# Kernel tuning notes

Hardware: AMD Instinct MI355X
Metric: run time of the kernel (lower is better)

## Reference

```python
import jax, jax.numpy as jnp
import numpy as np

# dims
B, T = 256, 64
N_AG, N_FEAT = 10, 4
X_DIM, X_PERM, X_STATIC = 44, 40, 10
HID, XEMB, NHID = 128, 32, 8
E = N_AG * (N_AG - 1)           # 90 directed edges (off-diagonal)
GEMB = NHID * E                 # 720 graph embedding per sample/step
RNN_IN = XEMB + 1 + GEMB        # 753
A_IN = X_STATIC + GEMB          # 730 (x_emb_size2==0 in GraphNN branch)
O_IN = XEMB + X_STATIC + 1 + GEMB  # 763

_off = np.ones((N_AG, N_AG)) - np.eye(N_AG)
RECV = jnp.asarray(np.where(_off)[0])  # rel_rec one-hot == gather by receiver idx
SEND = jnp.asarray(np.where(_off)[1])  # rel_send one-hot == gather by sender idx


def setup_inputs() -> dict:
    key = jax.random.key(0)
    ks = jax.random.split(key, 32)
    w = lambda k, shape: jax.random.normal(k, shape, jnp.float32) * 0.05
    return {
        'x': jax.random.normal(ks[0], (B, T + 1, X_DIM), jnp.float32),
        'x_demo': jax.random.normal(ks[1], (B, X_STATIC), jnp.float32),
        'f_treatment': jax.random.uniform(ks[2], (B, T + 1, 1), jnp.float32),
        'h0': jax.random.normal(ks[3], (B, HID), jnp.float32),
        # x2emb (Linear 4->32), x_static2emb (Linear 10->10)
        'W_x2emb': w(ks[4], (XEMB, X_DIM - X_PERM)), 'b_x2emb': w(ks[5], (XEMB,)),
        'W_stat': w(ks[6], (X_STATIC, X_STATIC)), 'b_stat': w(ks[7], (X_STATIC,)),
        # NRI-style MLP1 (node): 4->8->8 ; MLP2 (edge): 16->8->8
        'W_m1a': w(ks[8], (NHID, N_FEAT)), 'b_m1a': w(ks[9], (NHID,)),
        'W_m1b': w(ks[10], (NHID, NHID)), 'b_m1b': w(ks[11], (NHID,)),
        'W_m2a': w(ks[12], (NHID, 2 * NHID)), 'b_m2a': w(ks[13], (NHID,)),
        'W_m2b': w(ks[14], (NHID, NHID)), 'b_m2b': w(ks[15], (NHID,)),
        # treatment head: Linear(730->128)+ReLU, then Linear(128->1, no bias)
        'W_a1': w(ks[16], (HID, A_IN)), 'b_a1': w(ks[17], (HID,)),
        'W_a2': w(ks[18], (1, HID)),
        # outcome head: Linear(763->128)+ReLU, then Linear(128->1, no bias)
        'W_o1': w(ks[19], (HID, O_IN)), 'b_o1': w(ks[20], (HID,)),
        'W_o2': w(ks[21], (1, HID)),
        # GRUCell(753 -> 128)
        'W_ih': w(ks[22], (3 * HID, RNN_IN)), 'b_ih': w(ks[23], (3 * HID,)),
        'W_hh': w(ks[24], (3 * HID, HID)), 'b_hh': w(ks[25], (3 * HID,)),
    }


def reference(x, x_demo, f_treatment, h0, W_x2emb, b_x2emb, W_stat, b_stat,
              W_m1a, b_m1a, W_m1b, b_m1b, W_m2a, b_m2a, W_m2b, b_m2b,
              W_a1, b_a1, W_a2, W_o1, b_o1, W_o2, W_ih, b_ih, W_hh, b_hh):
    xt = x[:, :T]                       # (B,T,44); len_time = x.size(1)-1
    treat = f_treatment[:, :T]          # (B,T,1)
    demo = x_demo @ W_stat.T + b_stat   # (B,10) static embedding
    demoT = jnp.broadcast_to(demo[:, None], (B, T, X_STATIC))

    # --- GNN(x_permuted): mlp1 per node, node2edge gather, mlp2 per edge ---
    xa = xt[..., :X_PERM].reshape(B, T, N_AG, N_FEAT)
    h1 = jax.nn.elu(xa @ W_m1a.T + b_m1a)
    h1 = jax.nn.elu(h1 @ W_m1b.T + b_m1b)         # (B,T,N_AG,8); BN in eval = identity
    edges = jnp.concatenate([h1[:, :, RECV], h1[:, :, SEND]], axis=-1)  # (B,T,E,16)
    h2 = jax.nn.elu(edges @ W_m2a.T + b_m2a)
    h2 = jax.nn.elu(h2 @ W_m2b.T + b_m2b)         # (B,T,E,8)
    gemb = h2.reshape(B, T, GEMB)                 # (B,T,720)

    xemb = xt[..., X_PERM:] @ W_x2emb.T + b_x2emb  # (B,T,32)

    # --- treatment (a_or_ipw) head; dropout identity in eval ---
    a_in = jnp.concatenate([demoT, gemb], axis=-1)          # (B,T,730)
    a_out = jax.nn.relu(a_in @ W_a1.T + b_a1) @ W_a2.T      # (B,T,1)

    # --- outcome head ---
    o_in = jnp.concatenate([xemb, demoT, treat, gemb], axis=-1)  # (B,T,763)
    y_out = jax.nn.relu(o_in @ W_o1.T + b_o1) @ W_o2.T           # (B,T,1)

    # --- GRUCell recurrence over time ---
    rnn_in = jnp.concatenate([xemb, treat, gemb], axis=-1)  # (B,T,753)
    gi = rnn_in @ W_ih.T + b_ih                             # precompute input proj (B,T,3H)

    def step(h, g):
        gh = h @ W_hh.T + b_hh
        i_r, i_z, i_n = jnp.split(g, 3, axis=-1)
        h_r, h_z, h_n = jnp.split(gh, 3, axis=-1)
        r = jax.nn.sigmoid(i_r + h_r)
        z = jax.nn.sigmoid(i_z + h_z)
        n = jnp.tanh(i_n + r * h_n)
        h_new = (1.0 - z) * n + z * h
        return h_new, h_new

    _, hs = jax.lax.scan(step, h0, jnp.swapaxes(gi, 0, 1))
    hs = jnp.swapaxes(hs, 0, 1)                             # (B,T,128)

    return jnp.concatenate([a_out, y_out, hs], axis=-1)     # (B,T,130)
```

## Files before the change

kernel.cpp:

```cpp
#include <hip/hip_runtime.h>
#include <hip/hip_bf16.h>
#include <math.h>

#define BB     256
#define TT     64
#define BT     (BB*TT)
#define XD     44
#define XP     40
#define XS     10
#define HID    128
#define XEMB   32
#define NHID   8
#define NAG    10
#define NEDGE  90
#define GEMB   720
#define KF     768
#define NTOT   640


typedef __bf16  bf16_t;
typedef __bf16  bf16x4 __attribute__((ext_vector_type(4)));
typedef __bf16  bf16x8 __attribute__((ext_vector_type(8)));
typedef float   floatx4 __attribute__((ext_vector_type(4)));
typedef _Float16 half2_t __attribute__((ext_vector_type(2)));
typedef _Float16 half4_t __attribute__((ext_vector_type(4)));
typedef _Float16 half8_t __attribute__((ext_vector_type(8)));

__device__ __forceinline__ float rcp_fast(float x) { return __builtin_amdgcn_rcpf(x); }
__device__ __forceinline__ float sigmoid_fast(float v) { return rcp_fast(1.f + __expf(-v)); }
__device__ __forceinline__ float tanh_fast(float x) { return 1.f - 2.f * rcp_fast(1.f + __expf(2.f * x)); }
__device__ __forceinline__ float elu_fast(float v) { return v > 0.f ? v : __expf(v) - 1.f; }
__device__ __forceinline__ float fdot2f(half2_t a, half2_t b, float acc) {
  return __builtin_amdgcn_fdot2(a, b, acc, false);
}
__device__ __forceinline__ float dot8h(half8_t a, half8_t b, float acc) {
  acc = fdot2f(half2_t{a[0], a[1]}, half2_t{b[0], b[1]}, acc);
  acc = fdot2f(half2_t{a[2], a[3]}, half2_t{b[2], b[3]}, acc);
  acc = fdot2f(half2_t{a[4], a[5]}, half2_t{b[4], b[5]}, acc);
  acc = fdot2f(half2_t{a[6], a[7]}, half2_t{b[6], b[7]}, acc);
  return acc;
}
__device__ __forceinline__ void lds_barrier() {
  asm volatile("s_waitcnt lgkmcnt(0)" ::: "memory");
  __builtin_amdgcn_s_barrier();
}

__global__ __launch_bounds__(256) void prep_kernel(
    const float* __restrict__ Wa1, const float* __restrict__ ba1,
    const float* __restrict__ Wo1, const float* __restrict__ bo1,
    const float* __restrict__ Wih, const float* __restrict__ bih,
    bf16_t* __restrict__ WT, float* __restrict__ bcat) {
  int idx = blockIdx.x * 256 + threadIdx.x;
  if (idx >= NTOT * KF) return;
  int n = idx / KF, k = idx - n * KF;
  float v = 0.f;
  if (n < 128) {
    if (k >= 32 && k < 42)  v = Wa1[n * 730 + (k - 32)];
    else if (k >= 48)       v = Wa1[n * 730 + 10 + (k - 48)];
  } else if (n < 256) {
    int m = n - 128;
    if (k < 43)             v = Wo1[m * 763 + k];
    else if (k >= 48)       v = Wo1[m * 763 + 43 + (k - 48)];
  } else {
    int m = n - 256;
    if (k < 32)             v = Wih[m * 753 + k];
    else if (k == 42)       v = Wih[m * 753 + 32];
    else if (k >= 48)       v = Wih[m * 753 + 33 + (k - 48)];
  }
  WT[n * KF + k] = (bf16_t)v;
  if (k == 0) {
    bcat[n] = (n < 128) ? ba1[n] : (n < 256 ? bo1[n - 128] : bih[n - 256]);
  }
}

__global__ __launch_bounds__(64) void encoder_kernel(
    const float* __restrict__ x, const float* __restrict__ x_demo,
    const float* __restrict__ ftreat,
    const float* __restrict__ Wm1a, const float* __restrict__ bm1a,
    const float* __restrict__ Wm1b, const float* __restrict__ bm1b,
    const float* __restrict__ Wm2a, const float* __restrict__ bm2a,
    const float* __restrict__ Wm2b, const float* __restrict__ bm2b,
    const float* __restrict__ Wx2e, const float* __restrict__ bx2e,
    const float* __restrict__ Wst, const float* __restrict__ bst,
    bf16_t* __restrict__ F) {
  int blk = blockIdx.x;
  int b = blk >> 4, tc = blk & 15;
  int lane = threadIdx.x;

  __shared__ __align__(16) _Float16 h1sp[NAG * 8];
  __shared__ __align__(16) _Float16 w2aR[64];
  __shared__ __align__(16) _Float16 w2aS[64];
  __shared__ __align__(16) _Float16 w2bp[64];
  __shared__ float demoL[XS];

  if (lane < 8) {
    float4 v0 = *(const float4*)(Wm2a + lane * 16);
    float4 v1 = *(const float4*)(Wm2a + lane * 16 + 4);
    float4 v2 = *(const float4*)(Wm2a + lane * 16 + 8);
    float4 v3 = *(const float4*)(Wm2a + lane * 16 + 12);
    *(half8_t*)&w2aR[lane * 8] = half8_t{
        (_Float16)v0.x, (_Float16)v0.y, (_Float16)v0.z, (_Float16)v0.w,
        (_Float16)v1.x, (_Float16)v1.y, (_Float16)v1.z, (_Float16)v1.w};
    *(half8_t*)&w2aS[lane * 8] = half8_t{
        (_Float16)v2.x, (_Float16)v2.y, (_Float16)v2.z, (_Float16)v2.w,
        (_Float16)v3.x, (_Float16)v3.y, (_Float16)v3.z, (_Float16)v3.w};
    float4 u0 = *(const float4*)(Wm2b + lane * 8);
    float4 u1 = *(const float4*)(Wm2b + lane * 8 + 4);
    *(half8_t*)&w2bp[lane * 8] = half8_t{
        (_Float16)u0.x, (_Float16)u0.y, (_Float16)u0.z, (_Float16)u0.w,
        (_Float16)u1.x, (_Float16)u1.y, (_Float16)u1.z, (_Float16)u1.w};
  }
  if (lane < 10) {
    float s = bst[lane];
#pragma unroll
    for (int j = 0; j < 10; j++) s += x_demo[b * XS + j] * Wst[lane * 10 + j];
    demoL[lane] = s;
  }

  half4_t wA[8]; float bA[8];
  half8_t wB1[8]; float bB1[8];
  float bR[8], bG[8];
#pragma unroll
  for (int o = 0; o < 8; o++) {
    float4 v = *(const float4*)(Wm1a + o * 4);
    wA[o] = half4_t{(_Float16)v.x, (_Float16)v.y, (_Float16)v.z, (_Float16)v.w};
    bA[o] = bm1a[o];
    float4 w0 = *(const float4*)(Wm1b + o * 8);
    float4 w1 = *(const float4*)(Wm1b + o * 8 + 4);
    wB1[o] = half8_t{(_Float16)w0.x, (_Float16)w0.y, (_Float16)w0.z, (_Float16)w0.w,
                     (_Float16)w1.x, (_Float16)w1.y, (_Float16)w1.z, (_Float16)w1.w};
    bB1[o] = bm1b[o];
    bR[o] = bm2a[o];
    bG[o] = bm2b[o];
  }
  half4_t wX; float bX;
  {
    float4 v = *(const float4*)(Wx2e + (lane & 31) * 4);
    wX = half4_t{(_Float16)v.x, (_Float16)v.y, (_Float16)v.z, (_Float16)v.w};
    bX = bx2e[lane & 31];
  }
  __syncthreads();
  float demov = (lane >= 32 && lane < 42) ? demoL[lane - 32] : 0.f;

  for (int ti = 0; ti < 4; ti++) {
    int t = tc * 4 + ti;
    int tok = b * TT + t;
    const float* row = x + (size_t)(b * 65 + t) * XD;
    bf16_t* Frow = F + (size_t)tok * KF;

    if (lane < NAG) {
      float4 xa = *(const float4*)(row + lane * 4);
      half2_t x0{(_Float16)xa.x, (_Float16)xa.y};
      half2_t x1{(_Float16)xa.z, (_Float16)xa.w};
      float h1v[8];
#pragma unroll
      for (int o = 0; o < 8; o++) {
        float s = bA[o];
        s = fdot2f(x0, half2_t{wA[o][0], wA[o][1]}, s);
        s = fdot2f(x1, half2_t{wA[o][2], wA[o][3]}, s);
        h1v[o] = elu_fast(s);
      }
      half2_t e0{(_Float16)h1v[0], (_Float16)h1v[1]};
      half2_t e1{(_Float16)h1v[2], (_Float16)h1v[3]};
      half2_t e2{(_Float16)h1v[4], (_Float16)h1v[5]};
      half2_t e3{(_Float16)h1v[6], (_Float16)h1v[7]};
      half8_t hout;
#pragma unroll
      for (int o = 0; o < 8; o++) {
        float s = bB1[o];
        s = fdot2f(e0, half2_t{wB1[o][0], wB1[o][1]}, s);
        s = fdot2f(e1, half2_t{wB1[o][2], wB1[o][3]}, s);
        s = fdot2f(e2, half2_t{wB1[o][4], wB1[o][5]}, s);
        s = fdot2f(e3, half2_t{wB1[o][6], wB1[o][7]}, s);
        hout[o] = (_Float16)elu_fast(s);
      }
      *(half8_t*)&h1sp[lane * 8] = hout;
    }
    __syncthreads();

#pragma unroll
    for (int q = 0; q < 2; q++) {
      int e = lane + 64 * q;
      if (e < NEDGE) {
        int r = (e * 57) >> 9;
        int sd = e - 9 * r;
        sd += (sd >= r) ? 1 : 0;
        half8_t hr = *(const half8_t*)&h1sp[r * 8];
        half8_t hs = *(const half8_t*)&h1sp[sd * 8];
        float av[8];
#pragma unroll
        for (int o = 0; o < 8; o++) {
          half8_t wr8 = *(const half8_t*)&w2aR[o * 8];
          half8_t ws8 = *(const half8_t*)&w2aS[o * 8];
          float s = bR[o];
          s = dot8h(hr, wr8, s);
          s = dot8h(hs, ws8, s);
          av[o] = elu_fast(s);
        }
        half2_t a0{(_Float16)av[0], (_Float16)av[1]};
        half2_t a1{(_Float16)av[2], (_Float16)av[3]};
        half2_t a2{(_Float16)av[4], (_Float16)av[5]};
        half2_t a3{(_Float16)av[6], (_Float16)av[7]};
        union { bf16_t h[8]; uint4 u; } pk;
#pragma unroll
        for (int o = 0; o < 8; o++) {
          half8_t wb8 = *(const half8_t*)&w2bp[o * 8];
          float s = bG[o];
          s = fdot2f(a0, half2_t{wb8[0], wb8[1]}, s);
          s = fdot2f(a1, half2_t{wb8[2], wb8[3]}, s);
          s = fdot2f(a2, half2_t{wb8[4], wb8[5]}, s);
          s = fdot2f(a3, half2_t{wb8[6], wb8[7]}, s);
          pk.h[o] = (bf16_t)elu_fast(s);
        }
        *(uint4*)(Frow + 48 + e * 8) = pk.u;
      }
    }

    float4 xe = *(const float4*)(row + XP);
    if (lane < 32) {
      float s = bX;
      s = fdot2f(half2_t{(_Float16)xe.x, (_Float16)xe.y}, half2_t{wX[0], wX[1]}, s);
      s = fdot2f(half2_t{(_Float16)xe.z, (_Float16)xe.w}, half2_t{wX[2], wX[3]}, s);
      Frow[lane] = (bf16_t)s;
    } else if (lane < 42) {
      Frow[lane] = (bf16_t)demov;
    } else if (lane == 42) {
      Frow[42] = (bf16_t)ftreat[b * 65 + t];
    } else if (lane < 48) {
      Frow[lane] = (bf16_t)0.f;
    }
    __syncthreads();
  }
}

__global__ __launch_bounds__(256) void gemm_kernel(
    const bf16_t* __restrict__ F, const bf16_t* __restrict__ WT,
    const float* __restrict__ bcat, float* __restrict__ G) {
  __shared__ __align__(16) bf16_t As[128 * 32];
  __shared__ __align__(16) bf16_t Bs[128 * 32];

  int tid  = threadIdx.x;
  int lane = tid & 63;
  int wv   = tid >> 6;
  int wr   = wv >> 1, wc = wv & 1;
  int m0 = blockIdx.x * 128, n0 = blockIdx.y * 128;

  floatx4 acc[4][4];
#pragma unroll
  for (int i = 0; i < 4; i++)
#pragma unroll
    for (int j = 0; j < 4; j++) acc[i][j] = floatx4{0.f, 0.f, 0.f, 0.f};

  int c0 = tid, c1 = tid + 256;
  int r0 = c0 >> 2, p0 = c0 & 3;
  int r1 = c1 >> 2, p1 = c1 & 3;
  int qr = lane >> 4;
  int lr = lane & 15;

  for (int k0 = 0; k0 < KF; k0 += 32) {
    uint4 a0 = *(const uint4*)(F  + (size_t)(m0 + r0) * KF + k0 + p0 * 8);
    uint4 a1 = *(const uint4*)(F  + (size_t)(m0 + r1) * KF + k0 + p1 * 8);
    uint4 b0 = *(const uint4*)(WT + (size_t)(n0 + r0) * KF + k0 + p0 * 8);
    uint4 b1 = *(const uint4*)(WT + (size_t)(n0 + r1) * KF + k0 + p1 * 8);
    __syncthreads();
    ((uint4*)As)[c0] = a0; ((uint4*)As)[c1] = a1;
    ((uint4*)Bs)[c0] = b0; ((uint4*)Bs)[c1] = b1;
    __syncthreads();

    bf16x8 af[4], bf[4];
#pragma unroll
    for (int i = 0; i < 4; i++) {
      af[i] = *(const bf16x8*)(As + (wr * 64 + i * 16 + lr) * 32 + qr * 8);
      bf[i] = *(const bf16x8*)(Bs + (wc * 64 + i * 16 + lr) * 32 + qr * 8);
    }
#pragma unroll
    for (int i = 0; i < 4; i++)
#pragma unroll
      for (int j = 0; j < 4; j++)
        acc[i][j] = __builtin_amdgcn_mfma_f32_16x16x32_bf16(af[i], bf[j], acc[i][j], 0, 0, 0);
  }

#pragma unroll
  for (int i = 0; i < 4; i++) {
#pragma unroll
    for (int j = 0; j < 4; j++) {
      int col = n0 + wc * 64 + j * 16 + lr;
      float bv = bcat[col];
#pragma unroll
      for (int r = 0; r < 4; r++) {
        int row = m0 + wr * 64 + i * 16 + qr * 4 + r;
        G[(size_t)row * NTOT + col] = acc[i][j][r] + bv;
      }
    }
  }
}

__global__ __launch_bounds__(256) void head_kernel(
    const float* __restrict__ G, const float* __restrict__ Wa2,
    const float* __restrict__ Wo2, float* __restrict__ out) {
  int wid  = (blockIdx.x * 256 + threadIdx.x) >> 6;
  int lane = threadIdx.x & 63;
  const float* g = G + (size_t)wid * NTOT;
  float sa = fmaxf(g[lane], 0.f) * Wa2[lane] + fmaxf(g[lane + 64], 0.f) * Wa2[lane + 64];
  float sy = fmaxf(g[128 + lane], 0.f) * Wo2[lane] + fmaxf(g[192 + lane], 0.f) * Wo2[lane + 64];
#pragma unroll
  for (int off = 32; off > 0; off >>= 1) {
    sa += __shfl_down(sa, off, 64);
    sy += __shfl_down(sy, off, 64);
  }
  if (lane == 0) {
    out[(size_t)wid * 130 + 0] = sa;
    out[(size_t)wid * 130 + 1] = sy;
  }
}

__global__ __launch_bounds__(256, 1) void gru_kernel(
    const float* __restrict__ G, const float* __restrict__ h0,
    const float* __restrict__ Whh, const float* __restrict__ bhh,
    float* __restrict__ out) {
  int tid  = threadIdx.x;
  int w    = tid >> 6;
  int lane = tid & 63;
  int l15  = lane & 15;
  int quad = lane >> 4;
  int b0   = blockIdx.x * 16;
  int s    = b0 + l15;

  __shared__ __align__(16) bf16_t hT[2][16 * 136];

  bf16x8 afrag[6][4];
#pragma unroll
  for (int g = 0; g < 3; g++) {
#pragma unroll
    for (int tp = 0; tp < 2; tp++) {
      const float* wrow = Whh + (size_t)(g * 128 + w * 32 + tp * 16 + l15) * HID + quad * 8;
#pragma unroll
      for (int ks = 0; ks < 4; ks++) {
        float4 a = *(const float4*)(wrow + ks * 32);
        float4 b = *(const float4*)(wrow + ks * 32 + 4);
        afrag[g * 2 + tp][ks] = bf16x8{
            (bf16_t)a.x, (bf16_t)a.y, (bf16_t)a.z, (bf16_t)a.w,
            (bf16_t)b.x, (bf16_t)b.y, (bf16_t)b.z, (bf16_t)b.w};
      }
    }
  }
  int jb0 = w * 32 + quad * 4;
  int jb1 = jb0 + 16;
  floatx4 biasv[6];
#pragma unroll
  for (int g = 0; g < 3; g++) {
    biasv[g * 2 + 0] = *(const floatx4*)(bhh + g * 128 + jb0);
    biasv[g * 2 + 1] = *(const floatx4*)(bhh + g * 128 + jb1);
  }
  floatx4 hprev[2];
  hprev[0] = *(const floatx4*)(h0 + (size_t)s * HID + jb0);
  hprev[1] = *(const floatx4*)(h0 + (size_t)s * HID + jb1);

  {
    int sq = tid >> 4, u = (tid & 15) * 8;
    const float* hr = h0 + (size_t)(b0 + sq) * HID + u;
    float4 a = *(const float4*)hr;
    float4 b = *(const float4*)(hr + 4);
    *(bf16x8*)&hT[0][sq * 136 + u] = bf16x8{
        (bf16_t)a.x, (bf16_t)a.y, (bf16_t)a.z, (bf16_t)a.w,
        (bf16_t)b.x, (bf16_t)b.y, (bf16_t)b.z, (bf16_t)b.w};
  }
  const float* grow = G + (size_t)s * TT * NTOT;
  floatx4 gi[6];
#pragma unroll
  for (int g = 0; g < 3; g++) {
    gi[g * 2 + 0] = *(const floatx4*)(grow + 256 + g * 128 + jb0);
    gi[g * 2 + 1] = *(const floatx4*)(grow + 256 + g * 128 + jb1);
  }
  __syncthreads();

  float* obase = out + (size_t)s * TT * 130 + 2;

  for (int t = 0; t < TT; t++) {
    const bf16_t* hb = &hT[t & 1][l15 * 136 + quad * 8];
    bf16x8 bfrag[4];
#pragma unroll
    for (int ks = 0; ks < 4; ks++) bfrag[ks] = *(const bf16x8*)(hb + ks * 32);

    floatx4 ngi[6];
    if (t + 1 < TT) {
      const float* gn = grow + NTOT;
#pragma unroll
      for (int g = 0; g < 3; g++) {
        ngi[g * 2 + 0] = *(const floatx4*)(gn + 256 + g * 128 + jb0);
        ngi[g * 2 + 1] = *(const floatx4*)(gn + 256 + g * 128 + jb1);
      }
    }

    floatx4 acc[6];
#pragma unroll
    for (int i = 0; i < 6; i++) acc[i] = biasv[i];
#pragma unroll
    for (int ks = 0; ks < 4; ks++)
#pragma unroll
      for (int i = 0; i < 6; i++)
        acc[i] = __builtin_amdgcn_mfma_f32_16x16x32_bf16(afrag[i][ks], bfrag[ks], acc[i], 0, 0, 0);

#pragma unroll
    for (int tp = 0; tp < 2; tp++) {
      int jb = tp ? jb1 : jb0;
      floatx4 hn;
#pragma unroll
      for (int r = 0; r < 4; r++) {
        float rr = sigmoid_fast(gi[0 + tp][r] + acc[0 + tp][r]);
        float zz = sigmoid_fast(gi[2 + tp][r] + acc[2 + tp][r]);
        float nn = tanh_fast(gi[4 + tp][r] + rr * acc[4 + tp][r]);
        hn[r] = (1.f - zz) * nn + zz * hprev[tp][r];
      }
      hprev[tp] = hn;
      *(bf16x4*)&hT[(t + 1) & 1][l15 * 136 + jb] = bf16x4{
          (bf16_t)hn[0], (bf16_t)hn[1], (bf16_t)hn[2], (bf16_t)hn[3]};
      float* ob = obase + jb;
      *(float2*)ob       = float2{hn[0], hn[1]};
      *(float2*)(ob + 2) = float2{hn[2], hn[3]};
    }

    lds_barrier();
#pragma unroll
    for (int i = 0; i < 6; i++) gi[i] = ngi[i];
    grow  += NTOT;
    obase += 130;
  }
}

extern "C" void kernel_launch(void* const* d_in, const int* in_sizes, int n_in,
                              void* d_out, int out_size, void* d_ws, size_t ws_size,
                              hipStream_t stream) {
  const float* x      = (const float*)d_in[0];
  const float* x_demo = (const float*)d_in[1];
  const float* ftr    = (const float*)d_in[2];
  const float* h0     = (const float*)d_in[3];
  const float* Wx2e   = (const float*)d_in[4];
  const float* bx2e   = (const float*)d_in[5];
  const float* Wst    = (const float*)d_in[6];
  const float* bst    = (const float*)d_in[7];
  const float* Wm1a   = (const float*)d_in[8];
  const float* bm1a   = (const float*)d_in[9];
  const float* Wm1b   = (const float*)d_in[10];
  const float* bm1b   = (const float*)d_in[11];
  const float* Wm2a   = (const float*)d_in[12];
  const float* bm2a   = (const float*)d_in[13];
  const float* Wm2b   = (const float*)d_in[14];
  const float* bm2b   = (const float*)d_in[15];
  const float* Wa1    = (const float*)d_in[16];
  const float* ba1    = (const float*)d_in[17];
  const float* Wa2    = (const float*)d_in[18];
  const float* Wo1    = (const float*)d_in[19];
  const float* bo1    = (const float*)d_in[20];
  const float* Wo2    = (const float*)d_in[21];
  const float* Wih    = (const float*)d_in[22];
  const float* bih    = (const float*)d_in[23];
  const float* Whh    = (const float*)d_in[24];
  const float* bhh    = (const float*)d_in[25];
  float* out = (float*)d_out;

  char* ws = (char*)d_ws;
  bf16_t* F   = (bf16_t*)(ws);
  bf16_t* WT  = (bf16_t*)(ws + 25165824);
  float*  bc  = (float*)(ws + 25165824 + 983040);
  float*  G   = (float*)(ws + 25165824 + 983040 + 2560);

  prep_kernel<<<dim3((NTOT * KF + 255) / 256), dim3(256), 0, stream>>>(
      Wa1, ba1, Wo1, bo1, Wih, bih, WT, bc);
  encoder_kernel<<<dim3(BB * 16), dim3(64), 0, stream>>>(
      x, x_demo, ftr, Wm1a, bm1a, Wm1b, bm1b, Wm2a, bm2a, Wm2b, bm2b,
      Wx2e, bx2e, Wst, bst, F);
  gemm_kernel<<<dim3(BT / 128, NTOT / 128), dim3(256), 0, stream>>>(F, WT, bc, G);
  head_kernel<<<dim3(BT / 4), dim3(256), 0, stream>>>(G, Wa2, Wo2, out);
  gru_kernel<<<dim3(BB / 16), dim3(256), 0, stream>>>(G, h0, Whh, bhh, out);
}
```

Baseline: 263.3 us.

## Split GEMM output into head and time-major GRU buffers; widen GRU blocks to 512 threads

The GEMM epilogue now writes the head columns to a compact 256-wide buffer and the GRU input projection to a time-major [T][B][384] buffer. Each GRU step then reads a contiguous slab instead of striding through 640-wide rows. The GRU kernel doubles its threads to 512 (8 waves), so each wave handles 16 hidden units instead of 32, which halves per-wave MFMA and register work in the serial recurrence. It also unrolls the loop by two and prefetches gate inputs two steps ahead. The trade-offs are scattered, poorly coalesced stores in the GEMM epilogue and more barrier participants per step.

New measurement: 240.6 us. 8.6% less time.

```diff
diff --git a/kernel.cpp b/kernel.cpp
--- a/kernel.cpp
+++ b/kernel.cpp
@@ -235,7 +235,8 @@
 
 __global__ __launch_bounds__(256) void gemm_kernel(
     const bf16_t* __restrict__ F, const bf16_t* __restrict__ WT,
-    const float* __restrict__ bcat, float* __restrict__ G) {
+    const float* __restrict__ bcat, float* __restrict__ Gao,
+    float* __restrict__ Gih) {
   __shared__ __align__(16) bf16_t As[128 * 32];
   __shared__ __align__(16) bf16_t Bs[128 * 32];
 
@@ -289,18 +290,24 @@
 #pragma unroll
       for (int r = 0; r < 4; r++) {
         int row = m0 + wr * 64 + i * 16 + qr * 4 + r;
-        G[(size_t)row * NTOT + col] = acc[i][j][r] + bv;
+        float val = acc[i][j][r] + bv;
+        if (n0 < 256) {
+          Gao[(size_t)row * 256 + col] = val;
+        } else {
+          int tt = row & 63, bq = row >> 6;
+          Gih[(size_t)(tt * 256 + bq) * 384 + (col - 256)] = val;
+        }
       }
     }
   }
 }
 
 __global__ __launch_bounds__(256) void head_kernel(
-    const float* __restrict__ G, const float* __restrict__ Wa2,
+    const float* __restrict__ Gao, const float* __restrict__ Wa2,
     const float* __restrict__ Wo2, float* __restrict__ out) {
   int wid  = (blockIdx.x * 256 + threadIdx.x) >> 6;
   int lane = threadIdx.x & 63;
-  const float* g = G + (size_t)wid * NTOT;
+  const float* g = Gao + (size_t)wid * 256;
   float sa = fmaxf(g[lane], 0.f) * Wa2[lane] + fmaxf(g[lane + 64], 0.f) * Wa2[lane + 64];
   float sy = fmaxf(g[128 + lane], 0.f) * Wo2[lane] + fmaxf(g[192 + lane], 0.f) * Wo2[lane + 64];
 #pragma unroll
@@ -314,8 +321,8 @@
   }
 }
 
-__global__ __launch_bounds__(256, 1) void gru_kernel(
-    const float* __restrict__ G, const float* __restrict__ h0,
+__global__ __launch_bounds__(512, 1) void gru_kernel(
+    const float* __restrict__ Gih, const float* __restrict__ h0,
     const float* __restrict__ Whh, const float* __restrict__ bhh,
     float* __restrict__ out) {
   int tid  = threadIdx.x;
@@ -325,38 +332,29 @@
   int quad = lane >> 4;
   int b0   = blockIdx.x * 16;
   int s    = b0 + l15;
+  int jb   = w * 16 + quad * 4;
 
   __shared__ __align__(16) bf16_t hT[2][16 * 136];
 
-  bf16x8 afrag[6][4];
+  bf16x8 afrag[3][4];
 #pragma unroll
   for (int g = 0; g < 3; g++) {
-#pragma unroll
-    for (int tp = 0; tp < 2; tp++) {
-      const float* wrow = Whh + (size_t)(g * 128 + w * 32 + tp * 16 + l15) * HID + quad * 8;
-#pragma unroll
-      for (int ks = 0; ks < 4; ks++) {
-        float4 a = *(const float4*)(wrow + ks * 32);
-        float4 b = *(const float4*)(wrow + ks * 32 + 4);
-        afrag[g * 2 + tp][ks] = bf16x8{
-            (bf16_t)a.x, (bf16_t)a.y, (bf16_t)a.z, (bf16_t)a.w,
-            (bf16_t)b.x, (bf16_t)b.y, (bf16_t)b.z, (bf16_t)b.w};
-      }
-    }
-  }
-  int jb0 = w * 32 + quad * 4;
-  int jb1 = jb0 + 16;
-  floatx4 biasv[6];
-#pragma unroll
-  for (int g = 0; g < 3; g++) {
-    biasv[g * 2 + 0] = *(const floatx4*)(bhh + g * 128 + jb0);
-    biasv[g * 2 + 1] = *(const floatx4*)(bhh + g * 128 + jb1);
-  }
-  floatx4 hprev[2];
-  hprev[0] = *(const floatx4*)(h0 + (size_t)s * HID + jb0);
-  hprev[1] = *(const floatx4*)(h0 + (size_t)s * HID + jb1);
-
-  {
+    const float* wrow = Whh + (size_t)(g * 128 + w * 16 + l15) * HID + quad * 8;
+#pragma unroll
+    for (int ks = 0; ks < 4; ks++) {
+      float4 a = *(const float4*)(wrow + ks * 32);
+      float4 b = *(const float4*)(wrow + ks * 32 + 4);
+      afrag[g][ks] = bf16x8{
+          (bf16_t)a.x, (bf16_t)a.y, (bf16_t)a.z, (bf16_t)a.w,
+          (bf16_t)b.x, (bf16_t)b.y, (bf16_t)b.z, (bf16_t)b.w};
+    }
+  }
+  floatx4 biasv[3];
+#pragma unroll
+  for (int g = 0; g < 3; g++) biasv[g] = *(const floatx4*)(bhh + g * 128 + jb);
+  floatx4 hprev = *(const floatx4*)(h0 + (size_t)s * HID + jb);
+
+  if (tid < 256) {
     int sq = tid >> 4, u = (tid & 15) * 8;
     const float* hr = h0 + (size_t)(b0 + sq) * HID + u;
     float4 a = *(const float4*)hr;
@@ -365,67 +363,57 @@
         (bf16_t)a.x, (bf16_t)a.y, (bf16_t)a.z, (bf16_t)a.w,
         (bf16_t)b.x, (bf16_t)b.y, (bf16_t)b.z, (bf16_t)b.w};
   }
-  const float* grow = G + (size_t)s * TT * NTOT;
-  floatx4 gi[6];
-#pragma unroll
-  for (int g = 0; g < 3; g++) {
-    gi[g * 2 + 0] = *(const floatx4*)(grow + 256 + g * 128 + jb0);
-    gi[g * 2 + 1] = *(const floatx4*)(grow + 256 + g * 128 + jb1);
-  }
+
+  const float* gbase = Gih + (size_t)s * 384 + jb;
+  floatx4 gA[3], gB[3];
+#pragma unroll
+  for (int g = 0; g < 3; g++) gA[g] = *(const floatx4*)(gbase + g * 128);
+#pragma unroll
+  for (int g = 0; g < 3; g++) gB[g] = *(const floatx4*)(gbase + 98304 + g * 128);
   __syncthreads();
 
-  float* obase = out + (size_t)s * TT * 130 + 2;
-
-  for (int t = 0; t < TT; t++) {
-    const bf16_t* hb = &hT[t & 1][l15 * 136 + quad * 8];
-    bf16x8 bfrag[4];
-#pragma unroll
-    for (int ks = 0; ks < 4; ks++) bfrag[ks] = *(const bf16x8*)(hb + ks * 32);
-
-    floatx4 ngi[6];
-    if (t + 1 < TT) {
-      const float* gn = grow + NTOT;
-#pragma unroll
-      for (int g = 0; g < 3; g++) {
-        ngi[g * 2 + 0] = *(const floatx4*)(gn + 256 + g * 128 + jb0);
-        ngi[g * 2 + 1] = *(const floatx4*)(gn + 256 + g * 128 + jb1);
-      }
-    }
-
-    floatx4 acc[6];
-#pragma unroll
-    for (int i = 0; i < 6; i++) acc[i] = biasv[i];
-#pragma unroll
-    for (int ks = 0; ks < 4; ks++)
-#pragma unroll
-      for (int i = 0; i < 6; i++)
-        acc[i] = __builtin_amdgcn_mfma_f32_16x16x32_bf16(afrag[i][ks], bfrag[ks], acc[i], 0, 0, 0);
-
-#pragma unroll
-    for (int tp = 0; tp < 2; tp++) {
-      int jb = tp ? jb1 : jb0;
-      floatx4 hn;
-#pragma unroll
-      for (int r = 0; r < 4; r++) {
-        float rr = sigmoid_fast(gi[0 + tp][r] + acc[0 + tp][r]);
-        float zz = sigmoid_fast(gi[2 + tp][r] + acc[2 + tp][r]);
-        float nn = tanh_fast(gi[4 + tp][r] + rr * acc[4 + tp][r]);
-        hn[r] = (1.f - zz) * nn + zz * hprev[tp][r];
-      }
-      hprev[tp] = hn;
-      *(bf16x4*)&hT[(t + 1) & 1][l15 * 136 + jb] = bf16x4{
-          (bf16_t)hn[0], (bf16_t)hn[1], (bf16_t)hn[2], (bf16_t)hn[3]};
-      float* ob = obase + jb;
-      *(float2*)ob       = float2{hn[0], hn[1]};
-      *(float2*)(ob + 2) = float2{hn[2], hn[3]};
-    }
-
-    lds_barrier();
-#pragma unroll
-    for (int i = 0; i < 6; i++) gi[i] = ngi[i];
-    grow  += NTOT;
-    obase += 130;
-  }
+#define GRU_STEP(T, GREG)                                                      \
+  {                                                                            \
+    const bf16_t* hb = &hT[(T) & 1][l15 * 136 + quad * 8];                     \
+    bf16x8 bfrag[4];                                                           \
+    _Pragma("unroll")                                                          \
+    for (int ks = 0; ks < 4; ks++) bfrag[ks] = *(const bf16x8*)(hb + ks * 32); \
+    floatx4 acc[3];                                                            \
+    _Pragma("unroll")                                                          \
+    for (int g = 0; g < 3; g++) acc[g] = biasv[g];                             \
+    _Pragma("unroll")                                                          \
+    for (int ks = 0; ks < 4; ks++)                                             \
+      _Pragma("unroll")                                                        \
+      for (int g = 0; g < 3; g++)                                              \
+        acc[g] = __builtin_amdgcn_mfma_f32_16x16x32_bf16(                      \
+            afrag[g][ks], bfrag[ks], acc[g], 0, 0, 0);                         \
+    floatx4 hn;                                                                \
+    _Pragma("unroll")                                                          \
+    for (int r = 0; r < 4; r++) {                                              \
+      float rr = sigmoid_fast(GREG[0][r] + acc[0][r]);                         \
+      float zz = sigmoid_fast(GREG[1][r] + acc[1][r]);                         \
+      float nn = tanh_fast(GREG[2][r] + rr * acc[2][r]);                       \
+      hn[r] = (1.f - zz) * nn + zz * hprev[r];                                 \
+    }                                                                          \
+    hprev = hn;                                                                \
+    *(bf16x4*)&hT[((T) + 1) & 1][l15 * 136 + jb] =                             \
+        bf16x4{(bf16_t)hn[0], (bf16_t)hn[1], (bf16_t)hn[2], (bf16_t)hn[3]};    \
+    float* ob = out + ((size_t)s * TT + (T)) * 130 + 2 + jb;                   \
+    *(float2*)ob = float2{hn[0], hn[1]};                                       \
+    *(float2*)(ob + 2) = float2{hn[2], hn[3]};                                 \
+    if ((T) + 2 < TT) {                                                        \
+      const float* gp = gbase + (size_t)((T) + 2) * 98304;                     \
+      _Pragma("unroll")                                                        \
+      for (int g = 0; g < 3; g++) GREG[g] = *(const floatx4*)(gp + g * 128);   \
+    }                                                                          \
+    lds_barrier();                                                             \
+  }
+
+  for (int t = 0; t < TT; t += 2) {
+    GRU_STEP(t, gA);
+    GRU_STEP(t + 1, gB);
+  }
+#undef GRU_STEP
 }
 
 extern "C" void kernel_launch(void* const* d_in, const int* in_sizes, int n_in,
@@ -463,14 +451,15 @@
   bf16_t* F   = (bf16_t*)(ws);
   bf16_t* WT  = (bf16_t*)(ws + 25165824);
   float*  bc  = (float*)(ws + 25165824 + 983040);
-  float*  G   = (float*)(ws + 25165824 + 983040 + 2560);
+  float*  Gao = (float*)(ws + 25165824 + 983040 + 2560);
+  float*  Gih = (float*)(ws + 25165824 + 983040 + 2560 + 16777216);
 
   prep_kernel<<<dim3((NTOT * KF + 255) / 256), dim3(256), 0, stream>>>(
       Wa1, ba1, Wo1, bo1, Wih, bih, WT, bc);
   encoder_kernel<<<dim3(BB * 16), dim3(64), 0, stream>>>(
       x, x_demo, ftr, Wm1a, bm1a, Wm1b, bm1b, Wm2a, bm2a, Wm2b, bm2b,
       Wx2e, bx2e, Wst, bst, F);
-  gemm_kernel<<<dim3(BT / 128, NTOT / 128), dim3(256), 0, stream>>>(F, WT, bc, G);
-  head_kernel<<<dim3(BT / 4), dim3(256), 0, stream>>>(G, Wa2, Wo2, out);
-  gru_kernel<<<dim3(BB / 16), dim3(256), 0, stream>>>(G, h0, Whh, bhh, out);
-}
+  gemm_kernel<<<dim3(BT / 128, NTOT / 128), dim3(256), 0, stream>>>(F, WT, bc, Gao, Gih);
+  head_kernel<<<dim3(BT / 4), dim3(256), 0, stream>>>(Gao, Wa2, Wo2, out);
+  gru_kernel<<<dim3(BB / 16), dim3(512), 0, stream>>>(Gih, h0, Whh, bhh, out);
+}
```
